# Performance work log

Hardware: AMD Instinct MI355X
Metric: run time of the kernel (lower is better)

Reference implementation:

```python
import math
import jax, jax.numpy as jnp
import numpy as np

B, C, L = 16, 128, 2048


def setup_inputs() -> dict:
    key = jax.random.key(0)
    kq, kk, kv, km = jax.random.split(key, 4)
    proj_query = jax.random.normal(kq, (B, C, L), dtype=jnp.float32)
    proj_key = jax.random.normal(kk, (B, C, L), dtype=jnp.float32)
    proj_val = jax.random.normal(kv, (B, C, L), dtype=jnp.float32)
    padding_mask = (jax.random.uniform(km, (B, 1, L)) > 0.1).astype(jnp.float32)
    return {
        "proj_query": proj_query,
        "proj_key": proj_key,
        "proj_val": proj_val,
        "padding_mask": padding_mask,
    }


def reference(proj_query, proj_key, proj_val, padding_mask):
    c1 = proj_query.shape[1]
    # energy: [B, Lq, Lk]
    energy = jnp.einsum("bcq,bck->bqk", proj_query, proj_key)
    attention = energy / math.sqrt(c1)
    # additive log-mask before softmax (broadcast [B,1,Lk] -> [B,Lq,Lk])
    attention = attention + jnp.log(padding_mask + 1e-6)
    attention = jax.nn.softmax(attention, axis=-1)
    # multiplicative mask after softmax
    attention = attention * padding_mask
    # out = bmm(val [B,C,Lk], attention^T [B,Lk,Lq]) -> [B,C,Lq]
    out = jnp.einsum("bck,bqk->bcq", proj_val, attention)
    return out, jnp.transpose(attention, (0, 2, 1))
```

## Files before the change

kernel.cpp:

```cpp
#include <hip/hip_runtime.h>

#define B_ 16
#define C_ 128
#define L_ 2048

typedef unsigned short u16;
typedef __bf16 bf16x8 __attribute__((ext_vector_type(8)));
typedef float floatx4 __attribute__((ext_vector_type(4)));

static __device__ __forceinline__ u16 f_to_bf16(float f) {
    union { float f; unsigned int i; } v;
    v.f = f;
    unsigned int x = v.i;
    return (u16)((x + 0x7fffu + ((x >> 16) & 1u)) >> 16);
}
static __device__ __forceinline__ bf16x8 cvt8(floatx4 a, floatx4 b) {
    union { u16 u[8]; bf16x8 v; } p;
#pragma unroll
    for (int j = 0; j < 4; ++j) { p.u[j] = f_to_bf16(a[j]); p.u[4 + j] = f_to_bf16(b[j]); }
    return p.v;
}

__global__ void k_transpose(const float* __restrict__ X, u16* __restrict__ XT) {
    int t  = blockIdx.x * blockDim.x + threadIdx.x;
    int k  = t & (L_ - 1);
    int ch = (t >> 11) & 3;
    int b  = t >> 13;
    const float* src = X + (size_t)b * C_ * L_ + (size_t)(ch * 32) * L_ + k;
    u16* dst = XT + ((size_t)b * L_ + k) * C_ + ch * 32;
    u16 v[32];
#pragma unroll
    for (int c = 0; c < 32; ++c) v[c] = f_to_bf16(src[(size_t)c * L_]);
#pragma unroll
    for (int c = 0; c < 32; c += 8) {
        union { u16 u[8]; uint4 q; } p;
#pragma unroll
        for (int j = 0; j < 8; ++j) p.u[j] = v[c + j];
        *(uint4*)(dst + c) = p.q;
    }
}

#define BM 16
#define QS 136
#define LP 136

__launch_bounds__(1024, 1)
__global__ void k_fused(const float* __restrict__ Q, const u16* __restrict__ KT,
                        const float* __restrict__ V, const float* __restrict__ M,
                        float* __restrict__ PT, float* __restrict__ OUT) {
    __shared__ __attribute__((aligned(16))) u16 Qs[BM * QS];
    __shared__ __attribute__((aligned(16))) u16 Ps[16][BM * LP];
    __shared__ float redsum[BM][16];

    const int o       = blockIdx.x;
    const int logical = (o & 7) * 256 + (o >> 3);
    const int b       = logical >> 7;
    const int q0      = (logical & 127) * BM;

    const int tid  = threadIdx.x;
    const int lane = tid & 63;
    const int wave = tid >> 6;
    const int m16  = lane & 15;
    const int quad = lane >> 4;

    for (int i = tid; i < BM * C_; i += 1024) {
        int q = i & 15, c = i >> 4;
        Qs[q * QS + c] = f_to_bf16(Q[((size_t)b * C_ + c) * L_ + q0 + q]);
    }
    __syncthreads();

    bf16x8 afr[4];
#pragma unroll
    for (int f = 0; f < 4; ++f)
        afr[f] = *(const bf16x8*)(Qs + m16 * QS + f * 32 + quad * 8);

    const u16*   ktb = KT + (size_t)b * L_ * C_;
    const float* mb  = M + (size_t)b * L_;
    const float scale = 0.08838834764831845f;

    floatx4 accf[8];
    float rs[4] = {0.f, 0.f, 0.f, 0.f};
#pragma unroll
    for (int t = 0; t < 8; ++t) {
        const int kh = (wave << 7) + (t << 4);
        const u16* kr = ktb + (size_t)(kh + m16) * C_ + quad * 8;
        floatx4 s = {0.f, 0.f, 0.f, 0.f};
#pragma unroll
        for (int f = 0; f < 4; ++f)
            s = __builtin_amdgcn_mfma_f32_16x16x32_bf16(afr[f], *(const bf16x8*)(kr + f * 32), s, 0, 0, 0);
        const float lm = __logf(mb[kh + m16] + 1e-6f);
#pragma unroll
        for (int r = 0; r < 4; ++r) {
            const float e = __expf(fmaf(s[r], scale, lm));
            accf[t][r] = e;
            rs[r] += e;
        }
    }
#pragma unroll
    for (int r = 0; r < 4; ++r) {
        float v = rs[r];
        v += __shfl_xor(v, 1, 64);
        v += __shfl_xor(v, 2, 64);
        v += __shfl_xor(v, 4, 64);
        v += __shfl_xor(v, 8, 64);
        if (m16 == 0) redsum[quad * 4 + r][wave] = v;
    }
    __syncthreads();
    float rinv[4];
#pragma unroll
    for (int r = 0; r < 4; ++r) {
        const int q = quad * 4 + r;
        float v = redsum[q][0];
#pragma unroll
        for (int w = 1; w < 16; ++w) v += redsum[q][w];
        rinv[r] = 1.f / v;
    }

    float* ptb = PT + (size_t)b * L_ * L_ + q0;
    u16*   pw  = &Ps[wave][0];
#pragma unroll
    for (int t = 0; t < 8; ++t) {
        const int kh = (wave << 7) + (t << 4);
        const float mk = mb[kh + m16];
        floatx4 po;
#pragma unroll
        for (int r = 0; r < 4; ++r) po[r] = accf[t][r] * rinv[r] * mk;
        *(floatx4*)(ptb + (size_t)(kh + m16) * L_ + quad * 4) = po;
#pragma unroll
        for (int r = 0; r < 4; ++r)
            pw[(quad * 4 + r) * LP + (t << 4) + m16] = f_to_bf16(po[r]);
    }

    floatx4 acc[8];
#pragma unroll
    for (int ct = 0; ct < 8; ++ct) acc[ct] = (floatx4){0.f, 0.f, 0.f, 0.f};
    const float* vbb = V + (size_t)b * C_ * L_ + (wave << 7);
#pragma unroll
    for (int kt = 0; kt < 4; ++kt) {
        const bf16x8 pb = *(const bf16x8*)(pw + m16 * LP + (kt << 5) + quad * 8);
#pragma unroll
        for (int ct = 0; ct < 8; ++ct) {
            const float* va = vbb + (size_t)((ct << 4) + m16) * L_ + (kt << 5) + quad * 8;
            const bf16x8 a = cvt8(*(const floatx4*)(va), *(const floatx4*)(va + 4));
            acc[ct] = __builtin_amdgcn_mfma_f32_16x16x32_bf16(a, pb, acc[ct], 0, 0, 0);
        }
    }

    __syncthreads();
    floatx4* red = (floatx4*)&Ps[0][0];
    for (int half = 8; half >= 1; half >>= 1) {
        if (wave >= half && wave < 2 * half) {
            floatx4* slab = red + (size_t)(wave - half) * 512;
#pragma unroll
            for (int ct = 0; ct < 8; ++ct) slab[ct * 64 + lane] = acc[ct];
        }
        __syncthreads();
        if (wave < half) {
            floatx4* slab = red + (size_t)wave * 512;
#pragma unroll
            for (int ct = 0; ct < 8; ++ct) acc[ct] += slab[ct * 64 + lane];
        }
        __syncthreads();
    }

    if (wave == 0) {
        float* ob = OUT + (size_t)b * C_ * L_ + q0;
#pragma unroll
        for (int ct = 0; ct < 8; ++ct) {
            const int c0 = (ct << 4) + (quad << 2);
#pragma unroll
            for (int r = 0; r < 4; ++r)
                ob[(size_t)(c0 + r) * L_ + m16] = acc[ct][r];
        }
    }
}

extern "C" void kernel_launch(void* const* d_in, const int* in_sizes, int n_in,
                              void* d_out, int out_size, void* d_ws, size_t ws_size,
                              hipStream_t stream) {
    (void)in_sizes; (void)n_in; (void)out_size; (void)ws_size;
    const float* Q = (const float*)d_in[0];
    const float* K = (const float*)d_in[1];
    const float* V = (const float*)d_in[2];
    const float* M = (const float*)d_in[3];
    float* OUT = (float*)d_out;
    float* PT  = OUT + (size_t)B_ * C_ * L_;
    u16*   KT  = (u16*)d_ws;

    k_transpose<<<dim3((B_ * L_ * 4) / 256), dim3(256), 0, stream>>>(K, KT);
    k_fused<<<dim3(L_ / BM * B_), dim3(1024), 0, stream>>>(Q, KT, V, M, PT, OUT);
}
```

Baseline: 681.4 us.

## Double query tile to 32, interleave P writes with PV MMA, atomic LDS reduction

Each block now handles 32 query rows split across two wave groups, with each wave covering 256 keys, so every V element loaded from global memory feeds twice as many queries and the grid halves. The P-tile store and PV MFMA are interleaved per 32-key chunk using a small per-wave LDS buffer, and the log-reduction tree is replaced by LDS float atomics into an output accumulator. The log of the mask is replaced by a select between 0 and log(1e-6), and bf16 conversion of V uses packed hardware convert instructions. Risks include higher register pressure from 16 accumulator tiles, LDS atomic contention, and the mask shortcut assuming a strictly binary mask.

```diff
diff --git a/kernel.cpp b/kernel.cpp
--- a/kernel.cpp
+++ b/kernel.cpp
@@ -14,10 +14,12 @@
     unsigned int x = v.i;
     return (u16)((x + 0x7fffu + ((x >> 16) & 1u)) >> 16);
 }
-static __device__ __forceinline__ bf16x8 cvt8(floatx4 a, floatx4 b) {
-    union { u16 u[8]; bf16x8 v; } p;
-#pragma unroll
-    for (int j = 0; j < 4; ++j) { p.u[j] = f_to_bf16(a[j]); p.u[4 + j] = f_to_bf16(b[j]); }
+static __device__ __forceinline__ bf16x8 cvt8pk(floatx4 a, floatx4 b) {
+    union { unsigned int w[4]; bf16x8 v; } p;
+    asm("v_cvt_pk_bf16_f32 %0, %1, %2" : "=v"(p.w[0]) : "v"(a[0]), "v"(a[1]));
+    asm("v_cvt_pk_bf16_f32 %0, %1, %2" : "=v"(p.w[1]) : "v"(a[2]), "v"(a[3]));
+    asm("v_cvt_pk_bf16_f32 %0, %1, %2" : "=v"(p.w[2]) : "v"(b[0]), "v"(b[1]));
+    asm("v_cvt_pk_bf16_f32 %0, %1, %2" : "=v"(p.w[3]) : "v"(b[2]), "v"(b[3]));
     return p.v;
 }
 
@@ -40,55 +42,59 @@
     }
 }
 
-#define BM 16
+#define BM 32
 #define QS 136
-#define LP 136
+#define PS 36
 
 __launch_bounds__(1024, 1)
 __global__ void k_fused(const float* __restrict__ Q, const u16* __restrict__ KT,
                         const float* __restrict__ V, const float* __restrict__ M,
                         float* __restrict__ PT, float* __restrict__ OUT) {
     __shared__ __attribute__((aligned(16))) u16 Qs[BM * QS];
-    __shared__ __attribute__((aligned(16))) u16 Ps[16][BM * LP];
-    __shared__ float redsum[BM][16];
+    __shared__ __attribute__((aligned(16))) u16 Ps[16][16 * PS];
+    __shared__ float osum[C_ * BM];
+    __shared__ float redsum[BM][8];
 
     const int o       = blockIdx.x;
-    const int logical = (o & 7) * 256 + (o >> 3);
-    const int b       = logical >> 7;
-    const int q0      = (logical & 127) * BM;
+    const int logical = (o & 7) * 128 + (o >> 3);
+    const int b       = logical >> 6;
+    const int q0      = (logical & 63) * BM;
 
     const int tid  = threadIdx.x;
     const int lane = tid & 63;
     const int wave = tid >> 6;
     const int m16  = lane & 15;
     const int quad = lane >> 4;
+    const int qh   = wave >> 3;
+    const int ks   = wave & 7;
 
     for (int i = tid; i < BM * C_; i += 1024) {
-        int q = i & 15, c = i >> 4;
+        int q = i & 31, c = i >> 5;
         Qs[q * QS + c] = f_to_bf16(Q[((size_t)b * C_ + c) * L_ + q0 + q]);
     }
+    for (int i = tid; i < C_ * BM; i += 1024) osum[i] = 0.f;
     __syncthreads();
 
     bf16x8 afr[4];
 #pragma unroll
     for (int f = 0; f < 4; ++f)
-        afr[f] = *(const bf16x8*)(Qs + m16 * QS + f * 32 + quad * 8);
+        afr[f] = *(const bf16x8*)(Qs + (qh * 16 + m16) * QS + f * 32 + quad * 8);
 
     const u16*   ktb = KT + (size_t)b * L_ * C_;
     const float* mb  = M + (size_t)b * L_;
     const float scale = 0.08838834764831845f;
 
-    floatx4 accf[8];
+    floatx4 accf[16];
     float rs[4] = {0.f, 0.f, 0.f, 0.f};
 #pragma unroll
-    for (int t = 0; t < 8; ++t) {
-        const int kh = (wave << 7) + (t << 4);
+    for (int t = 0; t < 16; ++t) {
+        const int kh = (ks << 8) + (t << 4);
         const u16* kr = ktb + (size_t)(kh + m16) * C_ + quad * 8;
         floatx4 s = {0.f, 0.f, 0.f, 0.f};
 #pragma unroll
         for (int f = 0; f < 4; ++f)
             s = __builtin_amdgcn_mfma_f32_16x16x32_bf16(afr[f], *(const bf16x8*)(kr + f * 32), s, 0, 0, 0);
-        const float lm = __logf(mb[kh + m16] + 1e-6f);
+        const float lm = (mb[kh + m16] > 0.5f) ? 0.0f : -13.815511f;
 #pragma unroll
         for (int r = 0; r < 4; ++r) {
             const float e = __expf(fmaf(s[r], scale, lm));
@@ -103,75 +109,62 @@
         v += __shfl_xor(v, 2, 64);
         v += __shfl_xor(v, 4, 64);
         v += __shfl_xor(v, 8, 64);
-        if (m16 == 0) redsum[quad * 4 + r][wave] = v;
+        if (m16 == 0) redsum[qh * 16 + quad * 4 + r][ks] = v;
     }
     __syncthreads();
     float rinv[4];
 #pragma unroll
     for (int r = 0; r < 4; ++r) {
-        const int q = quad * 4 + r;
-        float v = redsum[q][0];
+        const int row = qh * 16 + quad * 4 + r;
+        float v = redsum[row][0];
 #pragma unroll
-        for (int w = 1; w < 16; ++w) v += redsum[q][w];
+        for (int w = 1; w < 8; ++w) v += redsum[row][w];
         rinv[r] = 1.f / v;
-    }
-
-    float* ptb = PT + (size_t)b * L_ * L_ + q0;
-    u16*   pw  = &Ps[wave][0];
-#pragma unroll
-    for (int t = 0; t < 8; ++t) {
-        const int kh = (wave << 7) + (t << 4);
-        const float mk = mb[kh + m16];
-        floatx4 po;
-#pragma unroll
-        for (int r = 0; r < 4; ++r) po[r] = accf[t][r] * rinv[r] * mk;
-        *(floatx4*)(ptb + (size_t)(kh + m16) * L_ + quad * 4) = po;
-#pragma unroll
-        for (int r = 0; r < 4; ++r)
-            pw[(quad * 4 + r) * LP + (t << 4) + m16] = f_to_bf16(po[r]);
     }
 
     floatx4 acc[8];
 #pragma unroll
     for (int ct = 0; ct < 8; ++ct) acc[ct] = (floatx4){0.f, 0.f, 0.f, 0.f};
-    const float* vbb = V + (size_t)b * C_ * L_ + (wave << 7);
+    float*       ptb = PT + (size_t)b * L_ * L_ + q0 + qh * 16;
+    u16*         pw  = &Ps[wave][0];
+    const float* vbb = V + (size_t)b * C_ * L_ + (ks << 8);
+
 #pragma unroll
-    for (int kt = 0; kt < 4; ++kt) {
-        const bf16x8 pb = *(const bf16x8*)(pw + m16 * LP + (kt << 5) + quad * 8);
+    for (int w = 0; w < 8; ++w) {
+#pragma unroll
+        for (int h = 0; h < 2; ++h) {
+            const int t  = 2 * w + h;
+            const int kh = (ks << 8) + (t << 4);
+            const float mk = mb[kh + m16];
+            floatx4 po;
+#pragma unroll
+            for (int r = 0; r < 4; ++r) po[r] = accf[t][r] * rinv[r] * mk;
+            *(floatx4*)(ptb + (size_t)(kh + m16) * L_ + quad * 4) = po;
+#pragma unroll
+            for (int r = 0; r < 4; ++r)
+                pw[(quad * 4 + r) * PS + h * 16 + m16] = f_to_bf16(po[r]);
+        }
+        const bf16x8 pb = *(const bf16x8*)(pw + m16 * PS + quad * 8);
+        const float* va = vbb + (w << 5) + quad * 8;
 #pragma unroll
         for (int ct = 0; ct < 8; ++ct) {
-            const float* va = vbb + (size_t)((ct << 4) + m16) * L_ + (kt << 5) + quad * 8;
-            const bf16x8 a = cvt8(*(const floatx4*)(va), *(const floatx4*)(va + 4));
+            const float* vp = va + (size_t)((ct << 4) + m16) * L_;
+            const bf16x8 a = cvt8pk(*(const floatx4*)vp, *(const floatx4*)(vp + 4));
             acc[ct] = __builtin_amdgcn_mfma_f32_16x16x32_bf16(a, pb, acc[ct], 0, 0, 0);
         }
     }
 
+#pragma unroll
+    for (int ct = 0; ct < 8; ++ct)
+#pragma unroll
+        for (int r = 0; r < 4; ++r)
+            atomicAdd(&osum[(ct * 16 + quad * 4 + r) * BM + qh * 16 + m16], acc[ct][r]);
     __syncthreads();
-    floatx4* red = (floatx4*)&Ps[0][0];
-    for (int half = 8; half >= 1; half >>= 1) {
-        if (wave >= half && wave < 2 * half) {
-            floatx4* slab = red + (size_t)(wave - half) * 512;
-#pragma unroll
-            for (int ct = 0; ct < 8; ++ct) slab[ct * 64 + lane] = acc[ct];
-        }
-        __syncthreads();
-        if (wave < half) {
-            floatx4* slab = red + (size_t)wave * 512;
-#pragma unroll
-            for (int ct = 0; ct < 8; ++ct) acc[ct] += slab[ct * 64 + lane];
-        }
-        __syncthreads();
-    }
 
-    if (wave == 0) {
-        float* ob = OUT + (size_t)b * C_ * L_ + q0;
-#pragma unroll
-        for (int ct = 0; ct < 8; ++ct) {
-            const int c0 = (ct << 4) + (quad << 2);
-#pragma unroll
-            for (int r = 0; r < 4; ++r)
-                ob[(size_t)(c0 + r) * L_ + m16] = acc[ct][r];
-        }
+    float* ob = OUT + (size_t)b * C_ * L_ + q0;
+    for (int i = tid; i < C_ * BM; i += 1024) {
+        int c = i >> 5, q = i & 31;
+        ob[(size_t)c * L_ + q] = osum[i];
     }
 }
 
```

Measured after the change: 868.3 us. 1.27x slower.
